# Kernel optimization log

Measured on AMD Instinct MI355X. Metric: run time of the kernel, lower is better.

Reference implementation:

```python
import jax, jax.numpy as jnp
import numpy as np

HID = 2048
N_HEADS = 16
N_KV = 16
HEAD_DIM = HID // N_HEADS
N_EXP = 8
TOP_K = 2
MOE_I = 1408
SH_I = 5632
EPS = 1e-6
ROPE_THETA = 1e6


def _rms(x, w):
    v = jnp.mean(jnp.square(x), axis=-1, keepdims=True)
    return (x * jax.lax.rsqrt(v + EPS)) * w


def _rope(q, k):
    # q, k: [B, S, H, D]
    S, D = q.shape[1], q.shape[-1]
    inv = 1.0 / (ROPE_THETA ** (jnp.arange(0, D, 2, dtype=jnp.float32) / D))
    freqs = jnp.arange(S, dtype=jnp.float32)[:, None] * inv[None, :]   # [S, D/2]
    emb = jnp.concatenate([freqs, freqs], axis=-1)                      # [S, D]
    cos = jnp.cos(emb)[None, :, None, :]
    sin = jnp.sin(emb)[None, :, None, :]
    def rot(t):
        t1, t2 = t[..., : D // 2], t[..., D // 2:]
        return jnp.concatenate([-t2, t1], axis=-1)
    return q * cos + rot(q) * sin, k * cos + rot(k) * sin


def setup_inputs() -> dict:
    key = jax.random.key(0)
    ks = jax.random.split(key, 20)
    s = 0.02
    d = {
        "x": jax.random.normal(ks[0], (2, 1024, HID), jnp.float32),
        "w_ln1": jnp.ones((HID,), jnp.float32),
        "wq": jax.random.normal(ks[1], (HID, N_HEADS * HEAD_DIM), jnp.float32) * s,
        "bq": jnp.zeros((N_HEADS * HEAD_DIM,), jnp.float32),
        "wk": jax.random.normal(ks[2], (HID, N_KV * HEAD_DIM), jnp.float32) * s,
        "bk": jnp.zeros((N_KV * HEAD_DIM,), jnp.float32),
        "wv": jax.random.normal(ks[3], (HID, N_KV * HEAD_DIM), jnp.float32) * s,
        "bv": jnp.zeros((N_KV * HEAD_DIM,), jnp.float32),
        "wo": jax.random.normal(ks[4], (N_HEADS * HEAD_DIM, HID), jnp.float32) * s,
        "w_ln2": jnp.ones((HID,), jnp.float32),
        "w_router": jax.random.normal(ks[5], (HID, N_EXP), jnp.float32) * s,
        "w_gate_e": jax.random.normal(ks[6], (N_EXP, HID, MOE_I), jnp.float32) * s,
        "w_up_e": jax.random.normal(ks[7], (N_EXP, HID, MOE_I), jnp.float32) * s,
        "w_down_e": jax.random.normal(ks[8], (N_EXP, MOE_I, HID), jnp.float32) * s,
        "w_sh_gate": jax.random.normal(ks[9], (HID, SH_I), jnp.float32) * s,
        "w_sh_up": jax.random.normal(ks[10], (HID, SH_I), jnp.float32) * s,
        "w_sh_down": jax.random.normal(ks[11], (SH_I, HID), jnp.float32) * s,
        "w_sh_eg": jax.random.normal(ks[12], (HID, 1), jnp.float32) * s,
    }
    return d


def reference(x, w_ln1, wq, bq, wk, bk, wv, bv, wo, w_ln2, w_router,
              w_gate_e, w_up_e, w_down_e, w_sh_gate, w_sh_up, w_sh_down, w_sh_eg):
    B, S, H = x.shape
    # ---- self-attention (pre-norm) ----
    h = _rms(x, w_ln1)
    q = (h @ wq + bq).reshape(B, S, N_HEADS, HEAD_DIM)
    k = (h @ wk + bk).reshape(B, S, N_KV, HEAD_DIM)
    v = (h @ wv + bv).reshape(B, S, N_KV, HEAD_DIM)
    q, k = _rope(q, k)
    rep = N_HEADS // N_KV
    if rep > 1:
        k = jnp.repeat(k, rep, axis=2)
        v = jnp.repeat(v, rep, axis=2)
    scores = jnp.einsum("bqhd,bkhd->bhqk", q, k) * (HEAD_DIM ** -0.5)
    causal = jnp.tril(jnp.ones((S, S), bool))
    scores = jnp.where(causal[None, None], scores, jnp.finfo(scores.dtype).min)
    attn = jax.nn.softmax(scores, axis=-1)
    ctx = jnp.einsum("bhqk,bkhd->bqhd", attn, v).reshape(B, S, N_HEADS * HEAD_DIM)
    x = x + ctx @ wo

    # ---- sparse MoE FFN (pre-norm) ----
    h = _rms(x, w_ln2).reshape(B * S, H)                     # [T, H]
    logits = h @ w_router                                     # [T, E]
    probs = jax.nn.softmax(logits, axis=-1)
    top_w, top_i = jax.lax.top_k(probs, TOP_K)               # norm_topk_prob=False
    combine = jnp.sum(jax.nn.one_hot(top_i, N_EXP, dtype=h.dtype)
                      * top_w[..., None], axis=1)            # [T, E]
    # dense per-expert compute combined with routing weights (same math as
    # the sorted grouped-GEMM dispatch in Qwen2MoeMLPStack)
    g = jnp.einsum("th,ehi->eti", h, w_gate_e)               # [E, T, I]
    u = jnp.einsum("th,ehi->eti", h, w_up_e)
    y = jnp.einsum("eti,eih->eth", jax.nn.silu(g) * u, w_down_e)
    routed = jnp.einsum("eth,te->th", y, combine)            # [T, H]
    # shared expert with sigmoid gate
    sh = (jax.nn.silu(h @ w_sh_gate) * (h @ w_sh_up)) @ w_sh_down
    sh = sh * jax.nn.sigmoid(h @ w_sh_eg)
    x = x + (routed + sh).reshape(B, S, H)
    return x
```

## Files before the change

### kernel.cpp

```cpp
#include <hip/hip_runtime.h>
#include <hip/hip_bf16.h>
#include <math.h>

#define TOKENS 2048
#define HIDDEN 2048
#define NH 16
#define HD 128
#define SEQ 1024
#define MOE_I 1408
#define SH_I 5632
#define K3 6144
#define MAXROWS 5120

typedef __hip_bfloat16 bf16;
typedef short bf16x8 __attribute__((ext_vector_type(8)));
typedef short bf16x4 __attribute__((ext_vector_type(4)));
typedef float f32x4 __attribute__((ext_vector_type(4)));
typedef float f32x16 __attribute__((ext_vector_type(16)));

__device__ __forceinline__ float b2f(bf16 x) { return __bfloat162float(x); }
__device__ __forceinline__ bf16 f2b(float x) { return __float2bfloat16(x); }
__device__ __forceinline__ void split2(float v, short& hi, short& lo) {
    bf16 h = f2b(v);
    bf16 l = f2b(v - b2f(h));
    hi = __builtin_bit_cast(short, h); lo = __builtin_bit_cast(short, l);
}

__device__ __forceinline__ void load_lds16(const void* g, void* l) {
    __builtin_amdgcn_global_load_lds(
        (const __attribute__((address_space(1))) unsigned int*)g,
        (__attribute__((address_space(3))) unsigned int*)l, 16, 0, 0);
}

__global__ __launch_bounds__(256) void rmsnorm3_k(
    const float* __restrict__ x, const float* __restrict__ w, bf16* __restrict__ out)
{
    const int row = blockIdx.x, tid = threadIdx.x;
    const float4* xr = (const float4*)(x + (size_t)row * HIDDEN);
    float4 v1 = xr[tid], v2 = xr[tid + 256];
    float ss = v1.x*v1.x + v1.y*v1.y + v1.z*v1.z + v1.w*v1.w
             + v2.x*v2.x + v2.y*v2.y + v2.z*v2.z + v2.w*v2.w;
    #pragma unroll
    for (int off = 1; off < 64; off <<= 1) ss += __shfl_xor(ss, off);
    __shared__ float ps[4];
    if ((tid & 63) == 0) ps[tid >> 6] = ss;
    __syncthreads();
    float tot = ps[0] + ps[1] + ps[2] + ps[3];
    float r = rsqrtf(tot * (1.0f / HIDDEN) + 1e-6f);
    bf16* o = out + (size_t)row * 4096;
    float vv[8] = {v1.x, v1.y, v1.z, v1.w, v2.x, v2.y, v2.z, v2.w};
    int idx[8]  = {tid*4, tid*4+1, tid*4+2, tid*4+3,
                   1024+tid*4, 1024+tid*4+1, 1024+tid*4+2, 1024+tid*4+3};
    #pragma unroll
    for (int u = 0; u < 8; u++) {
        short hi, lo; split2(vv[u] * r * w[idx[u]], hi, lo);
        o[idx[u]]        = __builtin_bit_cast(bf16, hi);
        o[2048 + idx[u]] = __builtin_bit_cast(bf16, lo);
    }
}

__global__ __launch_bounds__(256) void transpose_wz(
    const float* __restrict__ W, bf16* __restrict__ Wt, int K, int N,
    int nOff, long zsrc, long zdst)
{
    __shared__ float t[32][33];
    W  += (size_t)blockIdx.z * zsrc;
    Wt += (size_t)blockIdx.z * zdst;
    const int n0 = blockIdx.x * 32, k0 = blockIdx.y * 32;
    const int tx = threadIdx.x & 31, ty = threadIdx.x >> 5;
    #pragma unroll
    for (int i = 0; i < 4; i++)
        t[ty + i*8][tx] = W[(size_t)(k0 + ty + i*8) * N + n0 + tx];
    __syncthreads();
    #pragma unroll
    for (int i = 0; i < 4; i++)
        Wt[(size_t)(nOff + n0 + ty + i*8) * K + k0 + tx] = f2b(t[tx][ty + i*8]);
}

__global__ __launch_bounds__(256) void transpose_w3(
    const float* __restrict__ W, bf16* __restrict__ Wt2, int K, int N, int nOff)
{
    __shared__ float t[32][33];
    const int n0 = blockIdx.x * 32, k0 = blockIdx.y * 32;
    const int tx = threadIdx.x & 31, ty = threadIdx.x >> 5;
    #pragma unroll
    for (int i = 0; i < 4; i++)
        t[ty + i*8][tx] = W[(size_t)(k0 + ty + i*8) * N + n0 + tx];
    __syncthreads();
    #pragma unroll
    for (int i = 0; i < 4; i++) {
        float v = t[tx][ty + i*8];
        short hi, lo; split2(v, hi, lo);
        bf16* o = Wt2 + (size_t)(nOff + n0 + ty + i*8) * (2*K) + k0 + tx;
        o[0] = __builtin_bit_cast(bf16, hi);
        o[K] = __builtin_bit_cast(bf16, lo);
    }
}

__global__ __launch_bounds__(256) void gemm_bt(
    const bf16* __restrict__ A, const bf16* __restrict__ Bt,
    float* __restrict__ Cf, bf16* __restrict__ Cb, const float* __restrict__ bias,
    int M, int N, int K, int ldA, int ldB, int ldC, long zCstride, int limb3, int epi)
{
    __shared__ __align__(16) bf16 As[128 * 32];
    __shared__ __align__(16) bf16 Bs[128 * 32];
    const int tid = threadIdx.x;
    const int lane = tid & 63, wid = tid >> 6;
    const int l32 = lane & 31, lh2 = lane >> 5;
    const int wr = wid >> 1, wc = wid & 1;
    int lid = blockIdx.y * gridDim.x + blockIdx.x;
    {
        const int nwg = gridDim.x * gridDim.y;
        const int q = nwg >> 3, r = nwg & 7;
        const int xcd = lid & 7, idx = lid >> 3;
        lid = (xcd < r ? xcd * (q + 1) : r * (q + 1) + (xcd - r) * q) + idx;
    }
    const int m0 = (lid % gridDim.x) * 128, n0 = (lid / gridDim.x) * 128;
    const int f = tid * 8;
    const int r0 = f >> 5, c0 = f & 31;
    const int koff = blockIdx.z * K;

    f32x16 acc[2][2];
    #pragma unroll
    for (int m = 0; m < 2; m++)
        #pragma unroll
        for (int n = 0; n < 2; n++)
            #pragma unroll
            for (int j = 0; j < 16; j++) acc[m][n][j] = 0.f;

    const bf16* Ag0 = A + (size_t)(m0 + r0) * ldA + c0;
    const bf16* Ag1 = Ag0 + (size_t)64 * ldA;
    const bf16* Bg0 = Bt + (size_t)(n0 + r0) * ldB + c0;
    const bf16* Bg1 = Bg0 + (size_t)64 * ldB;

    for (int k0 = 0; k0 < K; k0 += 32) {
        const int kcat = koff + k0;
        int ka = kcat, kb = kcat;
        if (limb3) {
            ka = (kcat >= 4096) ? kcat - 4096 : kcat;
            kb = (kcat >= 2048) ? kcat - 2048 : kcat;
        }
        __syncthreads();
        load_lds16(Ag0 + ka, As + f);
        load_lds16(Ag1 + ka, As + f + 2048);
        load_lds16(Bg0 + kb, Bs + f);
        load_lds16(Bg1 + kb, Bs + f + 2048);
        __syncthreads();
        bf16x8 a[2][2], b[2][2];
        #pragma unroll
        for (int m = 0; m < 2; m++)
            #pragma unroll
            for (int kk = 0; kk < 2; kk++)
                a[m][kk] = *(const bf16x8*)&As[(wr*64 + m*32 + l32) * 32 + kk*16 + lh2*8];
        #pragma unroll
        for (int n = 0; n < 2; n++)
            #pragma unroll
            for (int kk = 0; kk < 2; kk++)
                b[n][kk] = *(const bf16x8*)&Bs[(wc*64 + n*32 + l32) * 32 + kk*16 + lh2*8];
        #pragma unroll
        for (int m = 0; m < 2; m++)
            #pragma unroll
            for (int n = 0; n < 2; n++)
                #pragma unroll
                for (int kk = 0; kk < 2; kk++)
                    acc[m][n] = __builtin_amdgcn_mfma_f32_32x32x16_bf16(a[m][kk], b[n][kk], acc[m][n], 0, 0, 0);
    }

    float* Cz = Cf + (size_t)blockIdx.z * zCstride;
    #pragma unroll
    for (int m = 0; m < 2; m++) {
        const int base_m = m0 + wr*64 + m*32 + 4*lh2;
        #pragma unroll
        for (int n = 0; n < 2; n++) {
            const int gcol = n0 + wc*64 + n*32 + l32;
            #pragma unroll
            for (int reg = 0; reg < 16; reg++) {
                const int grow = base_m + (reg & 3) + 8*(reg >> 2);
                const size_t o = (size_t)grow * ldC + gcol;
                const float v = acc[m][n][reg];
                if (epi == 0)      Cb[o] = f2b(v);
                else if (epi == 4) Cz[o] = v;
                else               Cf[o] = v + bias[gcol];
            }
        }
    }
}

__global__ __launch_bounds__(256) void gemm_gu(
    const bf16* __restrict__ A, const bf16* __restrict__ BtAll,
    const int* __restrict__ offc, const int* __restrict__ perm,
    bf16* __restrict__ C)
{
    const int e = blockIdx.z;
    const int off = offc[8 + e];
    const int padCnt = offc[9 + e] - off;
    const int m0 = blockIdx.x * 128;
    if (m0 >= padCnt) return;
    __shared__ __align__(16) bf16 As[128 * 32];
    __shared__ __align__(16) bf16 Bs[128 * 32];
    const int tid = threadIdx.x;
    const int lane = tid & 63, wid = tid >> 6;
    const int l32 = lane & 31, lh2 = lane >> 5;
    const int wr = wid >> 1, wc = wid & 1;
    const int n0 = blockIdx.y * 128;
    const int f = tid * 8;
    const int r0 = f >> 5, c0 = f & 31;
    const bf16* Bt = BtAll + (size_t)e * 2816 * 2048;

    int t0 = perm[off + m0 + r0];      if (t0 < 0) t0 = 0;
    int t1 = perm[off + m0 + r0 + 64]; if (t1 < 0) t1 = 0;

    f32x16 acc[2][2];
    #pragma unroll
    for (int m = 0; m < 2; m++)
        #pragma unroll
        for (int n = 0; n < 2; n++)
            #pragma unroll
            for (int j = 0; j < 16; j++) acc[m][n][j] = 0.f;

    const bf16* Ag0 = A + (size_t)t0 * 2048 + c0;
    const bf16* Ag1 = A + (size_t)t1 * 2048 + c0;
    const bf16* Bg0 = Bt + (size_t)(n0 + r0) * 2048 + c0;
    const bf16* Bg1 = Bg0 + (size_t)64 * 2048;

    for (int k0 = 0; k0 < 2048; k0 += 32) {
        __syncthreads();
        load_lds16(Ag0 + k0, As + f);
        load_lds16(Ag1 + k0, As + f + 2048);
        load_lds16(Bg0 + k0, Bs + f);
        load_lds16(Bg1 + k0, Bs + f + 2048);
        __syncthreads();
        bf16x8 a[2][2], b[2][2];
        #pragma unroll
        for (int m = 0; m < 2; m++)
            #pragma unroll
            for (int kk = 0; kk < 2; kk++)
                a[m][kk] = *(const bf16x8*)&As[(wr*64 + m*32 + l32) * 32 + kk*16 + lh2*8];
        #pragma unroll
        for (int n = 0; n < 2; n++)
            #pragma unroll
            for (int kk = 0; kk < 2; kk++)
                b[n][kk] = *(const bf16x8*)&Bs[(wc*64 + n*32 + l32) * 32 + kk*16 + lh2*8];
        #pragma unroll
        for (int m = 0; m < 2; m++)
            #pragma unroll
            for (int n = 0; n < 2; n++)
                #pragma unroll
                for (int kk = 0; kk < 2; kk++)
                    acc[m][n] = __builtin_amdgcn_mfma_f32_32x32x16_bf16(a[m][kk], b[n][kk], acc[m][n], 0, 0, 0);
    }

    #pragma unroll
    for (int m = 0; m < 2; m++) {
        const int base_m = m0 + wr*64 + m*32 + 4*lh2;
        #pragma unroll
        for (int n = 0; n < 2; n++) {
            const int gcol = n0 + wc*64 + n*32 + l32;
            #pragma unroll
            for (int reg = 0; reg < 16; reg++) {
                const int grow = base_m + (reg & 3) + 8*(reg >> 2);
                C[(size_t)(off + grow) * 2816 + gcol] = f2b(acc[m][n][reg]);
            }
        }
    }
}

__global__ __launch_bounds__(256) void gemm_down(
    const bf16* __restrict__ A, const bf16* __restrict__ BtAll,
    const int* __restrict__ offc, bf16* __restrict__ Y)
{
    const int e = blockIdx.z;
    const int off = offc[8 + e];
    const int padCnt = offc[9 + e] - off;
    const int m0 = blockIdx.x * 128;
    if (m0 >= padCnt) return;
    __shared__ __align__(16) bf16 As[128 * 32];
    __shared__ __align__(16) bf16 Bs[128 * 32];
    const int tid = threadIdx.x;
    const int lane = tid & 63, wid = tid >> 6;
    const int l32 = lane & 31, lh2 = lane >> 5;
    const int wr = wid >> 1, wc = wid & 1;
    const int n0 = blockIdx.y * 128;
    const int f = tid * 8;
    const int r0 = f >> 5, c0 = f & 31;
    const bf16* Bt = BtAll + (size_t)e * 2048 * 1408;

    f32x16 acc[2][2];
    #pragma unroll
    for (int m = 0; m < 2; m++)
        #pragma unroll
        for (int n = 0; n < 2; n++)
            #pragma unroll
            for (int j = 0; j < 16; j++) acc[m][n][j] = 0.f;

    const bf16* Ag0 = A + (size_t)(off + m0 + r0) * 1408 + c0;
    const bf16* Ag1 = Ag0 + (size_t)64 * 1408;
    const bf16* Bg0 = Bt + (size_t)(n0 + r0) * 1408 + c0;
    const bf16* Bg1 = Bg0 + (size_t)64 * 1408;

    for (int k0 = 0; k0 < 1408; k0 += 32) {
        __syncthreads();
        load_lds16(Ag0 + k0, As + f);
        load_lds16(Ag1 + k0, As + f + 2048);
        load_lds16(Bg0 + k0, Bs + f);
        load_lds16(Bg1 + k0, Bs + f + 2048);
        __syncthreads();
        bf16x8 a[2][2], b[2][2];
        #pragma unroll
        for (int m = 0; m < 2; m++)
            #pragma unroll
            for (int kk = 0; kk < 2; kk++)
                a[m][kk] = *(const bf16x8*)&As[(wr*64 + m*32 + l32) * 32 + kk*16 + lh2*8];
        #pragma unroll
        for (int n = 0; n < 2; n++)
            #pragma unroll
            for (int kk = 0; kk < 2; kk++)
                b[n][kk] = *(const bf16x8*)&Bs[(wc*64 + n*32 + l32) * 32 + kk*16 + lh2*8];
        #pragma unroll
        for (int m = 0; m < 2; m++)
            #pragma unroll
            for (int n = 0; n < 2; n++)
                #pragma unroll
                for (int kk = 0; kk < 2; kk++)
                    acc[m][n] = __builtin_amdgcn_mfma_f32_32x32x16_bf16(a[m][kk], b[n][kk], acc[m][n], 0, 0, 0);
    }

    #pragma unroll
    for (int m = 0; m < 2; m++) {
        const int base_m = m0 + wr*64 + m*32 + 4*lh2;
        #pragma unroll
        for (int n = 0; n < 2; n++) {
            const int gcol = n0 + wc*64 + n*32 + l32;
            #pragma unroll
            for (int reg = 0; reg < 16; reg++) {
                const int grow = base_m + (reg & 3) + 8*(reg >> 2);
                Y[(size_t)(off + grow) * 2048 + gcol] = f2b(acc[m][n][reg]);
            }
        }
    }
}

__global__ void rope_table_k(float2* __restrict__ cs)
{
    const int i = blockIdx.x * 256 + threadIdx.x;
    const int s = i >> 6, d = i & 63;
    const float fr = (float)s * powf(1.0e6f, -(float)d * (1.0f / 64.0f));
    float c, sn;
    sincosf(fr, &sn, &c);
    cs[i] = make_float2(c, sn);
}

__global__ void rope_f32_k(float* __restrict__ qkv, const float2* __restrict__ cs)
{
    const int idx = blockIdx.x * 256 + threadIdx.x;
    const int d  = idx & 63;
    const int hh = (idx >> 6) & 15;
    const size_t base = (size_t)(idx >> 10) * 6144 + hh * HD;
    const int s = (idx >> 10) & 1023;
    const float2 t = cs[(s << 6) | d];
    const float c = t.x, sn = t.y;
    float q0 = qkv[base + d], q1 = qkv[base + d + 64];
    qkv[base + d]      = q0 * c - q1 * sn;
    qkv[base + d + 64] = q1 * c + q0 * sn;
    float k0 = qkv[base + 2048 + d], k1 = qkv[base + 2048 + d + 64];
    qkv[base + 2048 + d]      = k0 * c - k1 * sn;
    qkv[base + 2048 + d + 64] = k1 * c + k0 * sn;
}

__global__ __launch_bounds__(256) void transpose_v3_k(
    const float* __restrict__ qkv, bf16* __restrict__ vth, bf16* __restrict__ vtl)
{
    __shared__ float t[32][33];
    const int s0 = blockIdx.x * 32, d0 = blockIdx.y * 32;
    const int bh = blockIdx.z, b = bh >> 4, h = bh & 15;
    const int tx = threadIdx.x & 31, ty = threadIdx.x >> 5;
    const float* vb = qkv + ((size_t)b * SEQ) * 6144 + 4096 + h * HD;
    #pragma unroll
    for (int i = 0; i < 4; i++)
        t[ty + i*8][tx] = vb[(size_t)(s0 + ty + i*8) * 6144 + d0 + tx];
    __syncthreads();
    const size_t ob = ((size_t)bh * HD) * SEQ;
    #pragma unroll
    for (int i = 0; i < 4; i++) {
        float val = t[tx][ty + i*8];
        short hi, lo; split2(val, hi, lo);
        const size_t o = ob + (size_t)(d0 + ty + i*8) * SEQ + s0 + tx;
        vth[o] = __builtin_bit_cast(bf16, hi);
        vtl[o] = __builtin_bit_cast(bf16, lo);
    }
}

__global__ __launch_bounds__(256) void attn3_k(
    const float* __restrict__ qkv,
    const bf16* __restrict__ vth, const bf16* __restrict__ vtl,
    bf16* __restrict__ ctx2)
{
    __shared__ __align__(16) bf16 Ksh[32 * 128], Ksl[32 * 128];
    __shared__ __align__(16) bf16 Vth[128 * 32], Vtl[128 * 32];
    __shared__ __align__(16) bf16 Ph[4][16 * 32], Pl[4][16 * 32];
    const int tid = threadIdx.x, lane = tid & 63, wid = tid >> 6;
    const int l16 = lane & 15, lh = lane >> 4;
    const int bh = blockIdx.y, b = bh >> 4, h = bh & 15;
    const int qbase = blockIdx.x * 64;
    const int qw = qbase + wid * 16;
    const float* qp = qkv + ((size_t)b * SEQ) * 6144 + h * HD;
    const float* kp = qkv + ((size_t)b * SEQ) * 6144 + 2048 + h * HD;
    const bf16* vph = vth + ((size_t)bh * HD) * SEQ;
    const bf16* vpl = vtl + ((size_t)bh * HD) * SEQ;

    bf16x8 aqh[4], aql[4];
    #pragma unroll
    for (int c = 0; c < 4; c++) {
        const float* qrow = qp + (size_t)(qw + l16) * 6144 + c*32 + lh*8;
        #pragma unroll
        for (int u = 0; u < 8; u++) {
            short hi, lo; split2(qrow[u], hi, lo);
            aqh[c][u] = hi; aql[c][u] = lo;
        }
    }

    f32x4 o[8];
    #pragma unroll
    for (int n = 0; n < 8; n++) o[n] = (f32x4){0.f, 0.f, 0.f, 0.f};
    float mj[4], lj[4];
    #pragma unroll
    for (int j = 0; j < 4; j++) { mj[j] = -1e30f; lj[j] = 0.f; }

    const int f = tid * 8;
    const int kr = tid >> 3, kc = (tid & 7) * 16;
    const int kt_end = qbase / 32 + 2;
    for (int kt = 0; kt < kt_end; ++kt) {
        const int kv0 = kt * 32;
        __syncthreads();
        {
            const float* krow = kp + (size_t)(kv0 + kr) * 6144 + kc;
            #pragma unroll
            for (int u = 0; u < 4; u++) {
                float4 kv4 = *(const float4*)(krow + u*4);
                short h0, l0, h1, l1, h2s, l2s, h3, l3;
                split2(kv4.x, h0, l0); split2(kv4.y, h1, l1);
                split2(kv4.z, h2s, l2s); split2(kv4.w, h3, l3);
                bf16x4 h4, l4;
                h4[0] = h0; h4[1] = h1; h4[2] = h2s; h4[3] = h3;
                l4[0] = l0; l4[1] = l1; l4[2] = l2s; l4[3] = l3;
                *(bf16x4*)&Ksh[kr*128 + kc + u*4] = h4;
                *(bf16x4*)&Ksl[kr*128 + kc + u*4] = l4;
            }
        }
        load_lds16(vph + (size_t)(f >> 5) * SEQ + kv0 + (f & 31), Vth + f);
        load_lds16(vph + (size_t)((f >> 5) + 64) * SEQ + kv0 + (f & 31), Vth + f + 2048);
        load_lds16(vpl + (size_t)(f >> 5) * SEQ + kv0 + (f & 31), Vtl + f);
        load_lds16(vpl + (size_t)((f >> 5) + 64) * SEQ + kv0 + (f & 31), Vtl + f + 2048);
        __syncthreads();

        f32x4 s0a = (f32x4){0.f,0.f,0.f,0.f}, s1a = (f32x4){0.f,0.f,0.f,0.f};
        #pragma unroll
        for (int c = 0; c < 4; c++) {
            bf16x8 bk0h = *(const bf16x8*)&Ksh[(l16) * 128 + c*32 + lh*8];
            bf16x8 bk0l = *(const bf16x8*)&Ksl[(l16) * 128 + c*32 + lh*8];
            bf16x8 bk1h = *(const bf16x8*)&Ksh[(l16 + 16) * 128 + c*32 + lh*8];
            bf16x8 bk1l = *(const bf16x8*)&Ksl[(l16 + 16) * 128 + c*32 + lh*8];
            s0a = __builtin_amdgcn_mfma_f32_16x16x32_bf16(aqh[c], bk0h, s0a, 0, 0, 0);
            s0a = __builtin_amdgcn_mfma_f32_16x16x32_bf16(aql[c], bk0h, s0a, 0, 0, 0);
            s0a = __builtin_amdgcn_mfma_f32_16x16x32_bf16(aqh[c], bk0l, s0a, 0, 0, 0);
            s1a = __builtin_amdgcn_mfma_f32_16x16x32_bf16(aqh[c], bk1h, s1a, 0, 0, 0);
            s1a = __builtin_amdgcn_mfma_f32_16x16x32_bf16(aql[c], bk1h, s1a, 0, 0, 0);
            s1a = __builtin_amdgcn_mfma_f32_16x16x32_bf16(aqh[c], bk1l, s1a, 0, 0, 0);
        }
        const float scale = 0.08838834764831845f;
        #pragma unroll
        for (int j = 0; j < 4; j++) {
            const int qrow = qw + lh*4 + j;
            float s0 = s0a[j] * scale, s1 = s1a[j] * scale;
            if (kv0 + l16 > qrow)      s0 = -1e30f;
            if (kv0 + l16 + 16 > qrow) s1 = -1e30f;
            float mx = fmaxf(s0, s1);
            #pragma unroll
            for (int off = 1; off < 16; off <<= 1) mx = fmaxf(mx, __shfl_xor(mx, off, 16));
            const float nm = fmaxf(mj[j], mx);
            const float al = __expf(mj[j] - nm);
            const float p0 = __expf(s0 - nm), p1 = __expf(s1 - nm);
            float rs = p0 + p1;
            #pragma unroll
            for (int off = 1; off < 16; off <<= 1) rs += __shfl_xor(rs, off, 16);
            lj[j] = lj[j] * al + rs;
            mj[j] = nm;
            #pragma unroll
            for (int n = 0; n < 8; n++) o[n][j] *= al;
            short h0, l0, h1, l1;
            split2(p0, h0, l0); split2(p1, h1, l1);
            Ph[wid][(lh*4 + j) * 32 + l16]      = __builtin_bit_cast(bf16, h0);
            Pl[wid][(lh*4 + j) * 32 + l16]      = __builtin_bit_cast(bf16, l0);
            Ph[wid][(lh*4 + j) * 32 + l16 + 16] = __builtin_bit_cast(bf16, h1);
            Pl[wid][(lh*4 + j) * 32 + l16 + 16] = __builtin_bit_cast(bf16, l1);
        }
        __syncthreads();
        const bf16x8 aph = *(const bf16x8*)&Ph[wid][l16 * 32 + lh*8];
        const bf16x8 apl = *(const bf16x8*)&Pl[wid][l16 * 32 + lh*8];
        #pragma unroll
        for (int n = 0; n < 8; n++) {
            bf16x8 bvh = *(const bf16x8*)&Vth[(n*16 + l16) * 32 + lh*8];
            bf16x8 bvl = *(const bf16x8*)&Vtl[(n*16 + l16) * 32 + lh*8];
            o[n] = __builtin_amdgcn_mfma_f32_16x16x32_bf16(aph, bvh, o[n], 0, 0, 0);
            o[n] = __builtin_amdgcn_mfma_f32_16x16x32_bf16(apl, bvh, o[n], 0, 0, 0);
            o[n] = __builtin_amdgcn_mfma_f32_16x16x32_bf16(aph, bvl, o[n], 0, 0, 0);
        }
    }

    float inv[4];
    #pragma unroll
    for (int j = 0; j < 4; j++) inv[j] = 1.0f / lj[j];
    #pragma unroll
    for (int n = 0; n < 8; n++)
        #pragma unroll
        for (int j = 0; j < 4; j++) {
            const float v = o[n][j] * inv[j];
            short hi, lo; split2(v, hi, lo);
            const size_t base = ((size_t)b * SEQ + (qw + lh*4 + j)) * 4096 + h * HD + n*16 + l16;
            ctx2[base]        = __builtin_bit_cast(bf16, hi);
            ctx2[base + 2048] = __builtin_bit_cast(bf16, lo);
        }
}

__global__ __launch_bounds__(256) void combine_rms_k(
    const float* __restrict__ x, const float* __restrict__ xp,
    const float* __restrict__ w, float* __restrict__ x1, bf16* __restrict__ h2)
{
    const int row = blockIdx.x, tid = threadIdx.x;
    const size_t rb = (size_t)row * HIDDEN;
    const long zs = (long)TOKENS * HIDDEN;
    float4 v[2];
    #pragma unroll
    for (int u = 0; u < 2; u++) {
        const int i = tid + u * 256;
        float4 a  = ((const float4*)(x + rb))[i];
        float4 p0 = ((const float4*)(xp + rb))[i];
        float4 p1 = ((const float4*)(xp + zs + rb))[i];
        float4 p2 = ((const float4*)(xp + 2*zs + rb))[i];
        v[u].x = a.x + p0.x + p1.x + p2.x;
        v[u].y = a.y + p0.y + p1.y + p2.y;
        v[u].z = a.z + p0.z + p1.z + p2.z;
        v[u].w = a.w + p0.w + p1.w + p2.w;
        ((float4*)(x1 + rb))[i] = v[u];
    }
    float ss = v[0].x*v[0].x + v[0].y*v[0].y + v[0].z*v[0].z + v[0].w*v[0].w
             + v[1].x*v[1].x + v[1].y*v[1].y + v[1].z*v[1].z + v[1].w*v[1].w;
    #pragma unroll
    for (int off = 1; off < 64; off <<= 1) ss += __shfl_xor(ss, off);
    __shared__ float ps[4];
    if ((tid & 63) == 0) ps[tid >> 6] = ss;
    __syncthreads();
    float tot = ps[0] + ps[1] + ps[2] + ps[3];
    float r = rsqrtf(tot * (1.0f / HIDDEN) + 1e-6f);
    #pragma unroll
    for (int u = 0; u < 2; u++) {
        const int i = (tid + u * 256) * 4;
        h2[rb + i]     = f2b(v[u].x * r * w[i]);
        h2[rb + i + 1] = f2b(v[u].y * r * w[i+1]);
        h2[rb + i + 2] = f2b(v[u].z * r * w[i+2]);
        h2[rb + i + 3] = f2b(v[u].w * r * w[i+3]);
    }
}

__global__ __launch_bounds__(256) void router_k(
    const float* __restrict__ x1, const float* __restrict__ wln,
    const float* __restrict__ wr, const float* __restrict__ weg,
    float* __restrict__ combine, float* __restrict__ sigeg)
{
    const int wid = threadIdx.x >> 6, lane = threadIdx.x & 63;
    const int t = blockIdx.x * 4 + wid;
    const float* xr = x1 + (size_t)t * HIDDEN;
    float ss = 0.f;
    for (int c = lane; c < HIDDEN; c += 64) { const float v = xr[c]; ss += v * v; }
    #pragma unroll
    for (int off = 1; off < 64; off <<= 1) ss += __shfl_xor(ss, off);
    const float r = rsqrtf(ss * (1.0f / HIDDEN) + 1e-6f);

    float acc[9];
    #pragma unroll
    for (int e = 0; e < 9; e++) acc[e] = 0.f;
    for (int c = lane; c < HIDDEN; c += 64) {
        const float hv = xr[c] * r * wln[c];
        const float* wrow = wr + (size_t)c * 8;
        #pragma unroll
        for (int e = 0; e < 8; e++) acc[e] += hv * wrow[e];
        acc[8] += hv * weg[c];
    }
    #pragma unroll
    for (int e = 0; e < 9; e++)
        #pragma unroll
        for (int off = 1; off < 64; off <<= 1) acc[e] += __shfl_xor(acc[e], off);
    float mx = acc[0];
    #pragma unroll
    for (int e = 1; e < 8; e++) mx = fmaxf(mx, acc[e]);
    float p[8], s = 0.f;
    #pragma unroll
    for (int e = 0; e < 8; e++) { p[e] = expf(acc[e] - mx); s += p[e]; }
    const float invs = 1.0f / s;
    #pragma unroll
    for (int e = 0; e < 8; e++) p[e] *= invs;
    int i1 = 0;
    #pragma unroll
    for (int e = 1; e < 8; e++) if (p[e] > p[i1]) i1 = e;
    int i2 = (i1 == 0) ? 1 : 0;
    #pragma unroll
    for (int e = 0; e < 8; e++) if (e != i1 && p[e] > p[i2]) i2 = e;
    if (lane < 8) combine[(size_t)t * 8 + lane] = (lane == i1 || lane == i2) ? p[lane] : 0.f;
    if (lane == 0) sigeg[t] = 1.0f / (1.0f + expf(-acc[8]));
}

__global__ __launch_bounds__(256) void count_fill_k(
    const float* __restrict__ comb, int* __restrict__ offc, int* __restrict__ perm,
    float* __restrict__ scale, int* __restrict__ inv)
{
    __shared__ int cnt[8], off[9], fil[8];
    const int tid = threadIdx.x;
    if (tid < 8) { cnt[tid] = 0; fil[tid] = 0; }
    __syncthreads();
    for (int t = tid; t < TOKENS; t += 256)
        #pragma unroll
        for (int e = 0; e < 8; e++)
            if (comb[(size_t)t * 8 + e] > 0.f) atomicAdd(&cnt[e], 1);
    __syncthreads();
    if (tid == 0) {
        off[0] = 0;
        for (int e = 0; e < 8; e++) off[e+1] = off[e] + ((cnt[e] + 127) & ~127);
    }
    __syncthreads();
    for (int i = tid; i < MAXROWS; i += 256) { perm[i] = -1; scale[i] = 0.f; }
    __syncthreads();
    for (int t = tid; t < TOKENS; t += 256) {
        int j = 0;
        #pragma unroll
        for (int e = 0; e < 8; e++) {
            const float c = comb[(size_t)t * 8 + e];
            if (c > 0.f) {
                int s = atomicAdd(&fil[e], 1);
                int slot = off[e] + s;
                perm[slot] = t;
                scale[slot] = c;
                inv[t * 2 + j] = slot;
                j++;
            }
        }
    }
    __syncthreads();
    if (tid < 9) offc[8 + tid] = off[tid];
}

__global__ void silu_k(const bf16* __restrict__ g, bf16* __restrict__ a,
                       const float* __restrict__ rowScale,
                       int I, int ldg, int rowsConst, const int* __restrict__ rowsPtr)
{
    const int idx = (blockIdx.x * 256 + threadIdx.x) * 4;
    const int rows = rowsPtr ? *rowsPtr : rowsConst;
    const int row = idx / I;
    if (row >= rows) return;
    const int col = idx - row * I;
    const float s = rowScale[row];
    const bf16* gr = g + (size_t)row * ldg + col;
    bf16* ar = a + (size_t)row * I + col;
    #pragma unroll
    for (int c = 0; c < 4; c++) {
        const float gv = b2f(gr[c]), uv = b2f(gr[I + c]);
        ar[c] = f2b(s * gv / (1.0f + __expf(-gv)) * uv);
    }
}

__global__ void final_k(const float* __restrict__ x1, const bf16* __restrict__ y,
                        const int* __restrict__ inv, const float* __restrict__ ysh,
                        float* __restrict__ out)
{
    const int i = blockIdx.x * 256 + threadIdx.x;
    const int t = i >> 9;
    const int col = (i & 511) * 4;
    const int s0 = inv[t*2], s1 = inv[t*2 + 1];
    const long zs = (long)TOKENS * HIDDEN;
    float4 a  = ((const float4*)x1)[i];
    float4 h0 = ((const float4*)ysh)[i];
    float4 h1 = ((const float4*)(ysh + zs))[i];
    const bf16* y0 = y + (size_t)s0 * 2048 + col;
    const bf16* y1 = y + (size_t)s1 * 2048 + col;
    float4 r;
    r.x = a.x + h0.x + h1.x + b2f(y0[0]) + b2f(y1[0]);
    r.y = a.y + h0.y + h1.y + b2f(y0[1]) + b2f(y1[1]);
    r.z = a.z + h0.z + h1.z + b2f(y0[2]) + b2f(y1[2]);
    r.w = a.w + h0.w + h1.w + b2f(y0[3]) + b2f(y1[3]);
    ((float4*)out)[i] = r;
}

extern "C" void kernel_launch(void* const* d_in, const int* in_sizes, int n_in,
                              void* d_out, int out_size, void* d_ws, size_t ws_size,
                              hipStream_t stream)
{
    const float* x     = (const float*)d_in[0];
    const float* w_ln1 = (const float*)d_in[1];
    const float* wq    = (const float*)d_in[2];
    const float* bq    = (const float*)d_in[3];
    const float* wk    = (const float*)d_in[4];
    const float* bk    = (const float*)d_in[5];
    const float* wv    = (const float*)d_in[6];
    const float* bv    = (const float*)d_in[7];
    const float* wo    = (const float*)d_in[8];
    const float* w_ln2 = (const float*)d_in[9];
    const float* w_rt  = (const float*)d_in[10];
    const float* w_ge  = (const float*)d_in[11];
    const float* w_ue  = (const float*)d_in[12];
    const float* w_de  = (const float*)d_in[13];
    const float* w_sg  = (const float*)d_in[14];
    const float* w_su  = (const float*)d_in[15];
    const float* w_sd  = (const float*)d_in[16];
    const float* w_eg  = (const float*)d_in[17];
    float* out = (float*)d_out;
    (void)in_sizes; (void)n_in; (void)out_size; (void)ws_size;

    char* ws = (char*)d_ws;
    float* x1    = (float*)(ws + 0);
    bf16*  h2    = (bf16*)(ws + 16777216);
    float* comb  = (float*)(ws + 25165824);
    float* seg   = (float*)(ws + 25231360);
    int*   offc  = (int*)(ws + 25239552);
    float* scale = (float*)(ws + 25243648);
    int*   perm  = (int*)(ws + 25276416);
    int*   inv   = (int*)(ws + 25297920);
    float* bqkv  = (float*)(ws + 25314304);
    float2* ropecs = (float2*)(ws + 25338880);
    const size_t S = 25863168;
    bf16*  hcat  = (bf16*)(ws + S);
    bf16*  wtqkv = (bf16*)(ws + S + 16777216);
    float* qkvf  = (float*)(ws + S + 67108864);
    bf16*  vth   = (bf16*)(ws + S);
    bf16*  vtl   = (bf16*)(ws + S + 8388608);
    bf16*  ctx2  = (bf16*)(ws + S + 16777216);
    bf16*  wt3o  = (bf16*)(ws + S + 33554432);
    float* xp    = (float*)(ws + S + 50331648);
    bf16*  wtgu  = (bf16*)(ws + S);
    bf16*  gb    = (bf16*)(ws + S + 92274688);
    bf16*  ab    = (bf16*)(ws + S);
    bf16*  wtd   = (bf16*)(ws + S + 14417920);
    bf16*  ymoe  = (bf16*)(ws + S + 60555264);
    bf16*  wtshgu = (bf16*)(ws + S);
    bf16*  gsh    = (bf16*)(ws + S + 81526784);
    bf16*  ash    = (bf16*)(ws + S);
    bf16*  wtshd  = (bf16*)(ws + S + 23068672);
    float* ysh    = (float*)(ws + S + 81526784);

    rmsnorm3_k<<<TOKENS, 256, 0, stream>>>(x, w_ln1, hcat);
    (void)hipMemcpyAsync(bqkv,        bq, 8192, hipMemcpyDeviceToDevice, stream);
    (void)hipMemcpyAsync(bqkv + 2048, bk, 8192, hipMemcpyDeviceToDevice, stream);
    (void)hipMemcpyAsync(bqkv + 4096, bv, 8192, hipMemcpyDeviceToDevice, stream);
    rope_table_k<<<256, 256, 0, stream>>>(ropecs);

    transpose_w3<<<dim3(64, 64), 256, 0, stream>>>(wq, wtqkv, HIDDEN, HIDDEN, 0);
    transpose_w3<<<dim3(64, 64), 256, 0, stream>>>(wk, wtqkv, HIDDEN, HIDDEN, 2048);
    transpose_w3<<<dim3(64, 64), 256, 0, stream>>>(wv, wtqkv, HIDDEN, HIDDEN, 4096);
    gemm_bt<<<dim3(16, 48, 1), 256, 0, stream>>>(hcat, wtqkv, qkvf, nullptr, bqkv,
                                                 TOKENS, 6144, K3, 4096, 4096, 6144, 0, 1, 5);

    rope_f32_k<<<8192, 256, 0, stream>>>(qkvf, ropecs);
    transpose_v3_k<<<dim3(32, 4, 32), 256, 0, stream>>>(qkvf, vth, vtl);
    attn3_k<<<dim3(16, 32), 256, 0, stream>>>(qkvf, vth, vtl, ctx2);

    transpose_w3<<<dim3(64, 64), 256, 0, stream>>>(wo, wt3o, HIDDEN, HIDDEN, 0);
    gemm_bt<<<dim3(16, 16, 3), 256, 0, stream>>>(ctx2, wt3o, xp, nullptr, nullptr,
                                                 TOKENS, HIDDEN, 2048, 4096, 4096, 2048,
                                                 (long)TOKENS * HIDDEN, 1, 4);
    combine_rms_k<<<TOKENS, 256, 0, stream>>>(x, xp, w_ln2, x1, h2);

    router_k<<<TOKENS / 4, 256, 0, stream>>>(x1, w_ln2, w_rt, w_eg, comb, seg);
    count_fill_k<<<1, 256, 0, stream>>>(comb, offc, perm, scale, inv);

    transpose_wz<<<dim3(44, 64, 8), 256, 0, stream>>>(w_ge, wtgu, HIDDEN, MOE_I, 0,
                                                      (long)HIDDEN*MOE_I, (long)2816*HIDDEN);
    transpose_wz<<<dim3(44, 64, 8), 256, 0, stream>>>(w_ue, wtgu, HIDDEN, MOE_I, MOE_I,
                                                      (long)HIDDEN*MOE_I, (long)2816*HIDDEN);
    gemm_gu<<<dim3(MAXROWS/128, 22, 8), 256, 0, stream>>>(h2, wtgu, offc, perm, gb);
    silu_k<<<(MAXROWS * MOE_I) / 1024, 256, 0, stream>>>(gb, ab, scale, MOE_I, 2816, 0, offc + 16);
    transpose_wz<<<dim3(64, 44, 8), 256, 0, stream>>>(w_de, wtd, MOE_I, HIDDEN, 0,
                                                      (long)MOE_I*HIDDEN, (long)HIDDEN*MOE_I);
    gemm_down<<<dim3(MAXROWS/128, 16, 8), 256, 0, stream>>>(ab, wtd, offc, ymoe);

    transpose_wz<<<dim3(176, 64, 1), 256, 0, stream>>>(w_sg, wtshgu, HIDDEN, SH_I, 0, 0, 0);
    transpose_wz<<<dim3(176, 64, 1), 256, 0, stream>>>(w_su, wtshgu, HIDDEN, SH_I, SH_I, 0, 0);
    gemm_bt<<<dim3(16, 88, 1), 256, 0, stream>>>(h2, wtshgu, nullptr, gsh, nullptr,
                                                 TOKENS, 2*SH_I, HIDDEN, HIDDEN, HIDDEN, 2*SH_I, 0, 0, 0);
    silu_k<<<(TOKENS * SH_I) / 1024, 256, 0, stream>>>(gsh, ash, seg, SH_I, 2*SH_I, TOKENS, nullptr);
    transpose_wz<<<dim3(64, 176, 1), 256, 0, stream>>>(w_sd, wtshd, SH_I, HIDDEN, 0, 0, 0);
    gemm_bt<<<dim3(16, 16, 2), 256, 0, stream>>>(ash, wtshd, ysh, nullptr, nullptr,
                                                 TOKENS, HIDDEN, SH_I/2, SH_I, SH_I, 2048,
                                                 (long)TOKENS * HIDDEN, 0, 4);

    final_k<<<(TOKENS * HIDDEN) / 1024, 256, 0, stream>>>(x1, ymoe, inv, ysh, out);
}
```

Baseline: 1.155 ms.

## Double K-tile depth to 64 and XOR-swizzle LDS layout in GEMM kernels

```diff
diff --git a/kernel.cpp b/kernel.cpp
--- a/kernel.cpp
+++ b/kernel.cpp
@@ -102,8 +102,8 @@
     float* __restrict__ Cf, bf16* __restrict__ Cb, const float* __restrict__ bias,
     int M, int N, int K, int ldA, int ldB, int ldC, long zCstride, int limb3, int epi)
 {
-    __shared__ __align__(16) bf16 As[128 * 32];
-    __shared__ __align__(16) bf16 Bs[128 * 32];
+    __shared__ __align__(16) bf16 As[128 * 64];
+    __shared__ __align__(16) bf16 Bs[128 * 64];
     const int tid = threadIdx.x;
     const int lane = tid & 63, wid = tid >> 6;
     const int l32 = lane & 31, lh2 = lane >> 5;
@@ -116,10 +116,16 @@
         lid = (xcd < r ? xcd * (q + 1) : r * (q + 1) + (xcd - r) * q) + idx;
     }
     const int m0 = (lid % gridDim.x) * 128, n0 = (lid / gridDim.x) * 128;
-    const int f = tid * 8;
-    const int r0 = f >> 5, c0 = f & 31;
     const int koff = blockIdx.z * K;
 
+    int srow[4], sslot[4];
+    #pragma unroll
+    for (int i = 0; i < 4; i++) {
+        const int c = tid + 256*i;
+        srow[i]  = c >> 3;
+        sslot[i] = (((c & 7) ^ (srow[i] & 7)) << 3);
+    }
+
     f32x16 acc[2][2];
     #pragma unroll
     for (int m = 0; m < 2; m++)
@@ -128,12 +134,7 @@
             #pragma unroll
             for (int j = 0; j < 16; j++) acc[m][n][j] = 0.f;
 
-    const bf16* Ag0 = A + (size_t)(m0 + r0) * ldA + c0;
-    const bf16* Ag1 = Ag0 + (size_t)64 * ldA;
-    const bf16* Bg0 = Bt + (size_t)(n0 + r0) * ldB + c0;
-    const bf16* Bg1 = Bg0 + (size_t)64 * ldB;
-
-    for (int k0 = 0; k0 < K; k0 += 32) {
+    for (int k0 = 0; k0 < K; k0 += 64) {
         const int kcat = koff + k0;
         int ka = kcat, kb = kcat;
         if (limb3) {
@@ -141,28 +142,33 @@
             kb = (kcat >= 2048) ? kcat - 2048 : kcat;
         }
         __syncthreads();
-        load_lds16(Ag0 + ka, As + f);
-        load_lds16(Ag1 + ka, As + f + 2048);
-        load_lds16(Bg0 + kb, Bs + f);
-        load_lds16(Bg1 + kb, Bs + f + 2048);
+        #pragma unroll
+        for (int i = 0; i < 4; i++) {
+            load_lds16(A  + (size_t)(m0 + srow[i]) * ldA + ka + sslot[i], As + (tid + 256*i) * 8);
+            load_lds16(Bt + (size_t)(n0 + srow[i]) * ldB + kb + sslot[i], Bs + (tid + 256*i) * 8);
+        }
         __syncthreads();
-        bf16x8 a[2][2], b[2][2];
-        #pragma unroll
-        for (int m = 0; m < 2; m++)
-            #pragma unroll
-            for (int kk = 0; kk < 2; kk++)
-                a[m][kk] = *(const bf16x8*)&As[(wr*64 + m*32 + l32) * 32 + kk*16 + lh2*8];
-        #pragma unroll
-        for (int n = 0; n < 2; n++)
-            #pragma unroll
-            for (int kk = 0; kk < 2; kk++)
-                b[n][kk] = *(const bf16x8*)&Bs[(wc*64 + n*32 + l32) * 32 + kk*16 + lh2*8];
-        #pragma unroll
-        for (int m = 0; m < 2; m++)
-            #pragma unroll
-            for (int n = 0; n < 2; n++)
+        bf16x8 a[2][4], b[2][4];
+        #pragma unroll
+        for (int m = 0; m < 2; m++) {
+            const int r = wr*64 + m*32 + l32, rx = r & 7;
+            #pragma unroll
+            for (int kk = 0; kk < 4; kk++)
+                a[m][kk] = *(const bf16x8*)&As[r*64 + ((((kk<<1)|lh2) ^ rx) << 3)];
+        }
+        #pragma unroll
+        for (int n = 0; n < 2; n++) {
+            const int r = wc*64 + n*32 + l32, rx = r & 7;
+            #pragma unroll
+            for (int kk = 0; kk < 4; kk++)
+                b[n][kk] = *(const bf16x8*)&Bs[r*64 + ((((kk<<1)|lh2) ^ rx) << 3)];
+        }
+        #pragma unroll
+        for (int kk = 0; kk < 4; kk++)
+            #pragma unroll
+            for (int m = 0; m < 2; m++)
                 #pragma unroll
-                for (int kk = 0; kk < 2; kk++)
+                for (int n = 0; n < 2; n++)
                     acc[m][n] = __builtin_amdgcn_mfma_f32_32x32x16_bf16(a[m][kk], b[n][kk], acc[m][n], 0, 0, 0);
     }
 
@@ -196,19 +202,24 @@
     const int padCnt = offc[9 + e] - off;
     const int m0 = blockIdx.x * 128;
     if (m0 >= padCnt) return;
-    __shared__ __align__(16) bf16 As[128 * 32];
-    __shared__ __align__(16) bf16 Bs[128 * 32];
+    __shared__ __align__(16) bf16 As[128 * 64];
+    __shared__ __align__(16) bf16 Bs[128 * 64];
     const int tid = threadIdx.x;
     const int lane = tid & 63, wid = tid >> 6;
     const int l32 = lane & 31, lh2 = lane >> 5;
     const int wr = wid >> 1, wc = wid & 1;
     const int n0 = blockIdx.y * 128;
-    const int f = tid * 8;
-    const int r0 = f >> 5, c0 = f & 31;
     const bf16* Bt = BtAll + (size_t)e * 2816 * 2048;
 
-    int t0 = perm[off + m0 + r0];      if (t0 < 0) t0 = 0;
-    int t1 = perm[off + m0 + r0 + 64]; if (t1 < 0) t1 = 0;
+    int srow[4], sslot[4], tok[4];
+    #pragma unroll
+    for (int i = 0; i < 4; i++) {
+        const int c = tid + 256*i;
+        srow[i]  = c >> 3;
+        sslot[i] = (((c & 7) ^ (srow[i] & 7)) << 3);
+        int t = perm[off + m0 + srow[i]];
+        tok[i] = (t < 0) ? 0 : t;
+    }
 
     f32x16 acc[2][2];
     #pragma unroll
@@ -218,35 +229,35 @@
             #pragma unroll
             for (int j = 0; j < 16; j++) acc[m][n][j] = 0.f;
 
-    const bf16* Ag0 = A + (size_t)t0 * 2048 + c0;
-    const bf16* Ag1 = A + (size_t)t1 * 2048 + c0;
-    const bf16* Bg0 = Bt + (size_t)(n0 + r0) * 2048 + c0;
-    const bf16* Bg1 = Bg0 + (size_t)64 * 2048;
-
-    for (int k0 = 0; k0 < 2048; k0 += 32) {
+    for (int k0 = 0; k0 < 2048; k0 += 64) {
         __syncthreads();
-        load_lds16(Ag0 + k0, As + f);
-        load_lds16(Ag1 + k0, As + f + 2048);
-        load_lds16(Bg0 + k0, Bs + f);
-        load_lds16(Bg1 + k0, Bs + f + 2048);
+        #pragma unroll
+        for (int i = 0; i < 4; i++) {
+            load_lds16(A  + (size_t)tok[i] * 2048 + k0 + sslot[i], As + (tid + 256*i) * 8);
+            load_lds16(Bt + (size_t)(n0 + srow[i]) * 2048 + k0 + sslot[i], Bs + (tid + 256*i) * 8);
+        }
         __syncthreads();
-        bf16x8 a[2][2], b[2][2];
-        #pragma unroll
-        for (int m = 0; m < 2; m++)
-            #pragma unroll
-            for (int kk = 0; kk < 2; kk++)
-                a[m][kk] = *(const bf16x8*)&As[(wr*64 + m*32 + l32) * 32 + kk*16 + lh2*8];
-        #pragma unroll
-        for (int n = 0; n < 2; n++)
-            #pragma unroll
-            for (int kk = 0; kk < 2; kk++)
-                b[n][kk] = *(const bf16x8*)&Bs[(wc*64 + n*32 + l32) * 32 + kk*16 + lh2*8];
-        #pragma unroll
-        for (int m = 0; m < 2; m++)
-            #pragma unroll
-            for (int n = 0; n < 2; n++)
+        bf16x8 a[2][4], b[2][4];
+        #pragma unroll
+        for (int m = 0; m < 2; m++) {
+            const int r = wr*64 + m*32 + l32, rx = r & 7;
+            #pragma unroll
+            for (int kk = 0; kk < 4; kk++)
+                a[m][kk] = *(const bf16x8*)&As[r*64 + ((((kk<<1)|lh2) ^ rx) << 3)];
+        }
+        #pragma unroll
+        for (int n = 0; n < 2; n++) {
+            const int r = wc*64 + n*32 + l32, rx = r & 7;
+            #pragma unroll
+            for (int kk = 0; kk < 4; kk++)
+                b[n][kk] = *(const bf16x8*)&Bs[r*64 + ((((kk<<1)|lh2) ^ rx) << 3)];
+        }
+        #pragma unroll
+        for (int kk = 0; kk < 4; kk++)
+            #pragma unroll
+            for (int m = 0; m < 2; m++)
                 #pragma unroll
-                for (int kk = 0; kk < 2; kk++)
+                for (int n = 0; n < 2; n++)
                     acc[m][n] = __builtin_amdgcn_mfma_f32_32x32x16_bf16(a[m][kk], b[n][kk], acc[m][n], 0, 0, 0);
     }
 
@@ -274,17 +285,23 @@
     const int padCnt = offc[9 + e] - off;
     const int m0 = blockIdx.x * 128;
     if (m0 >= padCnt) return;
-    __shared__ __align__(16) bf16 As[128 * 32];
-    __shared__ __align__(16) bf16 Bs[128 * 32];
+    __shared__ __align__(16) bf16 As[128 * 64];
+    __shared__ __align__(16) bf16 Bs[128 * 64];
     const int tid = threadIdx.x;
     const int lane = tid & 63, wid = tid >> 6;
     const int l32 = lane & 31, lh2 = lane >> 5;
     const int wr = wid >> 1, wc = wid & 1;
     const int n0 = blockIdx.y * 128;
-    const int f = tid * 8;
-    const int r0 = f >> 5, c0 = f & 31;
     const bf16* Bt = BtAll + (size_t)e * 2048 * 1408;
 
+    int srow[4], sslot[4];
+    #pragma unroll
+    for (int i = 0; i < 4; i++) {
+        const int c = tid + 256*i;
+        srow[i]  = c >> 3;
+        sslot[i] = (((c & 7) ^ (srow[i] & 7)) << 3);
+    }
+
     f32x16 acc[2][2];
     #pragma unroll
     for (int m = 0; m < 2; m++)
@@ -293,35 +310,35 @@
             #pragma unroll
             for (int j = 0; j < 16; j++) acc[m][n][j] = 0.f;
 
-    const bf16* Ag0 = A + (size_t)(off + m0 + r0) * 1408 + c0;
-    const bf16* Ag1 = Ag0 + (size_t)64 * 1408;
-    const bf16* Bg0 = Bt + (size_t)(n0 + r0) * 1408 + c0;
-    const bf16* Bg1 = Bg0 + (size_t)64 * 1408;
-
-    for (int k0 = 0; k0 < 1408; k0 += 32) {
+    for (int k0 = 0; k0 < 1408; k0 += 64) {
         __syncthreads();
-        load_lds16(Ag0 + k0, As + f);
-        load_lds16(Ag1 + k0, As + f + 2048);
-        load_lds16(Bg0 + k0, Bs + f);
-        load_lds16(Bg1 + k0, Bs + f + 2048);
+        #pragma unroll
+        for (int i = 0; i < 4; i++) {
+            load_lds16(A  + (size_t)(off + m0 + srow[i]) * 1408 + k0 + sslot[i], As + (tid + 256*i) * 8);
+            load_lds16(Bt + (size_t)(n0 + srow[i]) * 1408 + k0 + sslot[i], Bs + (tid + 256*i) * 8);
+        }
         __syncthreads();
-        bf16x8 a[2][2], b[2][2];
-        #pragma unroll
-        for (int m = 0; m < 2; m++)
-            #pragma unroll
-            for (int kk = 0; kk < 2; kk++)
-                a[m][kk] = *(const bf16x8*)&As[(wr*64 + m*32 + l32) * 32 + kk*16 + lh2*8];
-        #pragma unroll
-        for (int n = 0; n < 2; n++)
-            #pragma unroll
-            for (int kk = 0; kk < 2; kk++)
-                b[n][kk] = *(const bf16x8*)&Bs[(wc*64 + n*32 + l32) * 32 + kk*16 + lh2*8];
-        #pragma unroll
-        for (int m = 0; m < 2; m++)
-            #pragma unroll
-            for (int n = 0; n < 2; n++)
+        bf16x8 a[2][4], b[2][4];
+        #pragma unroll
+        for (int m = 0; m < 2; m++) {
+            const int r = wr*64 + m*32 + l32, rx = r & 7;
+            #pragma unroll
+            for (int kk = 0; kk < 4; kk++)
+                a[m][kk] = *(const bf16x8*)&As[r*64 + ((((kk<<1)|lh2) ^ rx) << 3)];
+        }
+        #pragma unroll
+        for (int n = 0; n < 2; n++) {
+            const int r = wc*64 + n*32 + l32, rx = r & 7;
+            #pragma unroll
+            for (int kk = 0; kk < 4; kk++)
+                b[n][kk] = *(const bf16x8*)&Bs[r*64 + ((((kk<<1)|lh2) ^ rx) << 3)];
+        }
+        #pragma unroll
+        for (int kk = 0; kk < 4; kk++)
+            #pragma unroll
+            for (int m = 0; m < 2; m++)
                 #pragma unroll
-                for (int kk = 0; kk < 2; kk++)
+                for (int n = 0; n < 2; n++)
                     acc[m][n] = __builtin_amdgcn_mfma_f32_32x32x16_bf16(a[m][kk], b[n][kk], acc[m][n], 0, 0, 0);
     }
 
```

New measurement: 1.025 ms. 11.3% less time.
